# Performance work log

Measured on AMD Instinct MI355X. Metric: run time of the kernel, lower is better.

The kernel has to match this reference:

```python
import jax, jax.numpy as jnp
import numpy as np

B, D, H, G, E = 32768, 256, 256, 8, 8  # batch, input_size, hidden_size, num_groups, experts_per_group


def setup_inputs() -> dict:
    key = jax.random.key(0)
    ks = jax.random.split(key, 5)
    s_d = 1.0 / np.sqrt(D)
    return {
        "x": jax.random.normal(ks[0], (B, D), dtype=jnp.float32),
        # gate: nn.Linear(D, G*E)
        "W_gate": jax.random.uniform(ks[1], (G * E, D), jnp.float32, -s_d, s_d),
        "b_gate": jax.random.uniform(ks[2], (G * E,), jnp.float32, -s_d, s_d),
        # experts: [G, E] x nn.Linear(D, H)
        "W_exp": jax.random.uniform(ks[3], (G, E, H, D), jnp.float32, -s_d, s_d),
        "b_exp": jax.random.uniform(ks[4], (G, E, H), jnp.float32, -s_d, s_d),
    }


def reference(x, W_gate, b_gate, W_exp, b_exp):
    # gate_outputs = softmax(gate(x), dim=1)  -> [B, G*E]
    gate = jax.nn.softmax(x @ W_gate.T + b_gate, axis=1)
    # per-group sum over experts of Linear(x): contract input dim i and expert dim e
    # [B, G, H]
    group_out = jnp.einsum("bi,gehi->bgh", x, W_exp) + b_exp.sum(axis=1)
    expert_flat = group_out.reshape(x.shape[0], -1)  # [B, G*H]
    # output = sum_g gate[b,g] * expert_flat[b,h]  == gate.sum(1) * expert_flat
    # (avoids materializing the [B, G*E, G*H] broadcast the torch code creates)
    out = gate.sum(axis=1, keepdims=True) * expert_flat
    return out
```

## Files before the change

### kernel.cpp

```cpp
#include <hip/hip_runtime.h>


typedef unsigned short u16;
typedef __bf16 bf16x8 __attribute__((ext_vector_type(8)));
typedef float f32x4 __attribute__((ext_vector_type(4)));

#define MB 32768
#define NN 2048
#define KK 256

__device__ __forceinline__ u16 f2bf(float f) {
    unsigned u = __builtin_bit_cast(unsigned, f);
    u += 0x7FFFu + ((u >> 16) & 1u);
    return (u16)(u >> 16);
}

__device__ __forceinline__ void gld16(const void* g, void* l) {
    __builtin_amdgcn_global_load_lds((const __attribute__((address_space(1))) void*)g,
                                     (__attribute__((address_space(3))) void*)l,
                                     16, 0, 0);
}

__global__ __launch_bounds__(256) void prep_kernel(
    const float* __restrict__ x, const float* __restrict__ Wexp,
    const float* __restrict__ bexp, u16* __restrict__ xb,
    u16* __restrict__ Ws, float* __restrict__ bs)
{
    const int blk = blockIdx.x;
    const int t = threadIdx.x;
    if (blk < 512) {
        const int tid = blk * 256 + t;
        const int n = tid >> 6;
        const int i = (tid & 63) << 2;
        const int g = n >> 8, h = n & 255;
        const float* base = Wexp + ((size_t)(g * 8) * 256 + h) * 256 + i;
        float s0 = 0.f, s1 = 0.f, s2 = 0.f, s3 = 0.f;
#pragma unroll
        for (int e = 0; e < 8; ++e) {
            const float4 v = *(const float4*)(base + (size_t)e * 65536);
            s0 += v.x; s1 += v.y; s2 += v.z; s3 += v.w;
        }
        ushort4 o;
        o.x = f2bf(s0); o.y = f2bf(s1); o.z = f2bf(s2); o.w = f2bf(s3);
        *(ushort4*)(Ws + (size_t)n * KK + i) = o;
        if ((tid & 63) == 0) {
            float sb = 0.f;
#pragma unroll
            for (int e = 0; e < 8; ++e) sb += bexp[(g * 8 + e) * 256 + h];
            bs[n] = sb;
        }
    } else {
        int idx = (blk - 512) * 256 + t;
        const float4* xv = (const float4*)x;
#pragma unroll
        for (int it = 0; it < 4; ++it) {
            const int j = idx + it * 524288;
            const float4 v = xv[j];
            ushort4 o;
            o.x = f2bf(v.x); o.y = f2bf(v.y); o.z = f2bf(v.z); o.w = f2bf(v.w);
            *(ushort4*)(xb + (size_t)j * 4) = o;
        }
    }
}

__global__ __launch_bounds__(256) void gemm_kernel(
    const u16* __restrict__ A, const u16* __restrict__ Bt,
    const float* __restrict__ bias, float* __restrict__ C)
{
    __shared__ __align__(16) u16 sA[128 * 32];
    __shared__ __align__(16) u16 sB[128 * 32];

    const int t = threadIdx.x;
    const int m0 = blockIdx.x * 128;
    const int n0 = blockIdx.y * 128;

    const int lane = t & 63;
    const int w = t >> 6;
    const int wm = (w & 1) << 6;
    const int wn = (w >> 1) << 6;
    const int lr = lane & 15;
    const int quad = lane >> 4;

    f32x4 acc[4][4] = {};

    const int srow = t >> 2;
    const int sk = (t & 3) << 3;
    const u16* Ag = A + (size_t)(m0 + srow) * KK + sk;
    const u16* Bg = Bt + (size_t)(n0 + srow) * KK + sk;
    u16* lA = sA + t * 8;
    u16* lB = sB + t * 8;

    for (int k0 = 0; k0 < KK; k0 += 32) {
        gld16(Ag + k0, lA);
        gld16(Ag + (size_t)64 * KK + k0, lA + 64 * 32);
        gld16(Bg + k0, lB);
        gld16(Bg + (size_t)64 * KK + k0, lB + 64 * 32);
        __syncthreads();

        bf16x8 af[4], bfr[4];
#pragma unroll
        for (int mi = 0; mi < 4; ++mi)
            af[mi] = *(const bf16x8*)(sA + (wm + mi * 16 + lr) * 32 + quad * 8);
#pragma unroll
        for (int ni = 0; ni < 4; ++ni)
            bfr[ni] = *(const bf16x8*)(sB + (wn + ni * 16 + lr) * 32 + quad * 8);
#pragma unroll
        for (int mi = 0; mi < 4; ++mi)
#pragma unroll
            for (int ni = 0; ni < 4; ++ni)
                acc[mi][ni] = __builtin_amdgcn_mfma_f32_16x16x32_bf16(
                    af[mi], bfr[ni], acc[mi][ni], 0, 0, 0);
        __syncthreads();
    }

#pragma unroll
    for (int ni = 0; ni < 4; ++ni) {
        const int col = n0 + wn + ni * 16 + lr;
        const float bv = bias[col];
#pragma unroll
        for (int mi = 0; mi < 4; ++mi) {
            const int row = m0 + wm + mi * 16 + quad * 4;
            float* Cp = C + (size_t)row * NN + col;
#pragma unroll
            for (int r = 0; r < 4; ++r)
                Cp[(size_t)r * NN] = acc[mi][ni][r] + bv;
        }
    }
}

extern "C" void kernel_launch(void* const* d_in, const int* in_sizes, int n_in,
                              void* d_out, int out_size, void* d_ws, size_t ws_size,
                              hipStream_t stream) {
    const float* x    = (const float*)d_in[0];
    const float* Wexp = (const float*)d_in[3];
    const float* bexp = (const float*)d_in[4];
    float* out = (float*)d_out;

    u16*   xb = (u16*)d_ws;
    u16*   Ws = (u16*)((char*)d_ws + (size_t)16777216);
    float* bs = (float*)((char*)d_ws + (size_t)16777216 + 1048576);

    prep_kernel<<<2560, 256, 0, stream>>>(x, Wexp, bexp, xb, Ws, bs);
    dim3 grid(MB / 128, NN / 128);
    gemm_kernel<<<grid, 256, 0, stream>>>(xb, Ws, bs, out);
}
```

Measured before the change: 368.9 us.

## Double K-tile depth, XOR-swizzle LDS, and reorder grid for A-tile reuse

The GEMM K-tile grows from 32 to 64, halving the number of barrier-separated iterations. The shared-memory layout gains an XOR swizzle on 16-byte chunks to avoid bank conflicts on fragment reads. The grid is transposed so consecutive blocks share the same A row-tile across N, improving L2 reuse of x, and launch bounds request 3 blocks per CU. The cost is more LDS per block, which could limit occupancy.

```diff
diff --git a/kernel.cpp b/kernel.cpp
--- a/kernel.cpp
+++ b/kernel.cpp
@@ -8,6 +8,7 @@
 #define MB 32768
 #define NN 2048
 #define KK 256
+#define BK 64
 
 __device__ __forceinline__ u16 f2bf(float f) {
     unsigned u = __builtin_bit_cast(unsigned, f);
@@ -63,16 +64,16 @@
     }
 }
 
-__global__ __launch_bounds__(256) void gemm_kernel(
+__global__ __launch_bounds__(256, 3) void gemm_kernel(
     const u16* __restrict__ A, const u16* __restrict__ Bt,
     const float* __restrict__ bias, float* __restrict__ C)
 {
-    __shared__ __align__(16) u16 sA[128 * 32];
-    __shared__ __align__(16) u16 sB[128 * 32];
+    __shared__ __align__(16) u16 sA[128 * BK];
+    __shared__ __align__(16) u16 sB[128 * BK];
 
     const int t = threadIdx.x;
-    const int m0 = blockIdx.x * 128;
-    const int n0 = blockIdx.y * 128;
+    const int n0 = blockIdx.x * 128;
+    const int m0 = blockIdx.y * 128;
 
     const int lane = t & 63;
     const int w = t >> 6;
@@ -83,33 +84,41 @@
 
     f32x4 acc[4][4] = {};
 
-    const int srow = t >> 2;
-    const int sk = (t & 3) << 3;
-    const u16* Ag = A + (size_t)(m0 + srow) * KK + sk;
-    const u16* Bg = Bt + (size_t)(n0 + srow) * KK + sk;
-    u16* lA = sA + t * 8;
-    u16* lB = sB + t * 8;
+    const int srow = t >> 3;
+    const int scs  = t & 7;
 
-    for (int k0 = 0; k0 < KK; k0 += 32) {
-        gld16(Ag + k0, lA);
-        gld16(Ag + (size_t)64 * KK + k0, lA + 64 * 32);
-        gld16(Bg + k0, lB);
-        gld16(Bg + (size_t)64 * KK + k0, lB + 64 * 32);
+    for (int k0 = 0; k0 < KK; k0 += BK) {
+#pragma unroll
+        for (int r = 0; r < 4; ++r) {
+            const int row = srow + r * 32;
+            const int gc  = ((scs ^ (row & 7)) << 3);
+            gld16(A  + (size_t)(m0 + row) * KK + k0 + gc, sA + (size_t)(r * 256 + t) * 8);
+            gld16(Bt + (size_t)(n0 + row) * KK + k0 + gc, sB + (size_t)(r * 256 + t) * 8);
+        }
         __syncthreads();
 
-        bf16x8 af[4], bfr[4];
 #pragma unroll
-        for (int mi = 0; mi < 4; ++mi)
-            af[mi] = *(const bf16x8*)(sA + (wm + mi * 16 + lr) * 32 + quad * 8);
+        for (int kk = 0; kk < 2; ++kk) {
+            bf16x8 af[4], bf[4];
 #pragma unroll
-        for (int ni = 0; ni < 4; ++ni)
-            bfr[ni] = *(const bf16x8*)(sB + (wn + ni * 16 + lr) * 32 + quad * 8);
+            for (int mi = 0; mi < 4; ++mi) {
+                const int rr = wm + mi * 16 + lr;
+                const int c  = (kk * 4 + quad) ^ (rr & 7);
+                af[mi] = *(const bf16x8*)(sA + rr * BK + (c << 3));
+            }
 #pragma unroll
-        for (int mi = 0; mi < 4; ++mi)
+            for (int ni = 0; ni < 4; ++ni) {
+                const int rr = wn + ni * 16 + lr;
+                const int c  = (kk * 4 + quad) ^ (rr & 7);
+                bf[ni] = *(const bf16x8*)(sB + rr * BK + (c << 3));
+            }
 #pragma unroll
-            for (int ni = 0; ni < 4; ++ni)
-                acc[mi][ni] = __builtin_amdgcn_mfma_f32_16x16x32_bf16(
-                    af[mi], bfr[ni], acc[mi][ni], 0, 0, 0);
+            for (int mi = 0; mi < 4; ++mi)
+#pragma unroll
+                for (int ni = 0; ni < 4; ++ni)
+                    acc[mi][ni] = __builtin_amdgcn_mfma_f32_16x16x32_bf16(
+                        af[mi], bf[ni], acc[mi][ni], 0, 0, 0);
+        }
         __syncthreads();
     }
 
@@ -141,6 +150,6 @@
     float* bs = (float*)((char*)d_ws + (size_t)16777216 + 1048576);
 
     prep_kernel<<<2560, 256, 0, stream>>>(x, Wexp, bexp, xb, Ws, bs);
-    dim3 grid(MB / 128, NN / 128);
+    dim3 grid(NN / 128, MB / 128);
     gemm_kernel<<<grid, 256, 0, stream>>>(xb, Ws, bs, out);
 }
```

Result: faster. 336.3 us (-8.8%).
